# Kernel tuning notes

Hardware: AMD Instinct MI355X
Metric: run time of the kernel (lower is better)

Reference implementation:

```python
import jax, jax.numpy as jnp
import numpy as np

N = 100000          # nodes
E = 1600000         # edges
F_IN = 128          # in_channels
C = 32              # hidden_channels (per head)
H = 4               # heads
NEG_SLOPE = 0.2     # PyG GATConv default leaky_relu slope


def setup_inputs() -> dict:
    key = jax.random.key(0)
    ks = jax.random.split(key, 6)
    x = jax.random.normal(ks[0], (N, F_IN), dtype=jnp.float32)
    edge_index = jax.random.randint(ks[1], (2, E), 0, N, dtype=jnp.int32)
    # learned params (PyG GATConv: lin weight, att_src, att_dst, bias)
    W = jax.random.normal(ks[2], (F_IN, H * C), dtype=jnp.float32) * (1.0 / np.sqrt(F_IN))
    att_src = jax.random.normal(ks[3], (H, C), dtype=jnp.float32) * 0.1
    att_dst = jax.random.normal(ks[4], (H, C), dtype=jnp.float32) * 0.1
    bias = jnp.zeros((H * C,), dtype=jnp.float32)
    return {"x": x, "edge_index": edge_index, "W": W,
            "att_src": att_src, "att_dst": att_dst, "bias": bias}


def reference(x, edge_index, W, att_src, att_dst, bias):
    # linear projection, split into heads: [N, H, C]
    h = (x @ W).reshape(N, H, C)
    # per-node attention terms: [N, H]
    a_src = jnp.einsum('nhc,hc->nh', h, att_src)
    a_dst = jnp.einsum('nhc,hc->nh', h, att_dst)
    src, dst = edge_index[0], edge_index[1]
    # edge-wise logits: [E, H]
    alpha = jax.nn.leaky_relu(a_src[src] + a_dst[dst], NEG_SLOPE)
    # segment softmax over incoming edges of each dst node
    amax = jax.ops.segment_max(alpha, dst, num_segments=N)       # [N, H]
    amax = jnp.where(jnp.isfinite(amax), amax, 0.0)
    ex = jnp.exp(alpha - amax[dst])                              # [E, H]
    denom = jax.ops.segment_sum(ex, dst, num_segments=N)         # [N, H]
    alpha = ex / (denom[dst] + 1e-16)                            # [E, H]
    # weighted messages, scatter-add to dst: [N, H, C]
    msg = h[src] * alpha[:, :, None]
    out = jax.ops.segment_sum(msg, dst, num_segments=N)
    out = out.reshape(N, H * C) + bias
    return jax.nn.elu(out)
```

## Files before the change

kernel.cpp:

```cpp
#include <hip/hip_runtime.h>
#include <hip/hip_bf16.h>
#include <math.h>

#define N_NODES 100000
#define N_EDGES 1600000
#define NEG_SLOPE 0.2f

#define NB_BUCKET 782
#define ST_CAP 2560

#define OFF_H     0
#define OFF_ASRC  25600000
#define OFF_ADST  27200000
#define OFF_OFFS  28800000
#define OFF_BCNT  29200128
#define OFF_BOFF  29204224
#define OFF_BCUR  29208320
#define OFF_TMP   29212416
#define OFF_CSR   35612416

__device__ __forceinline__ float leaky(float x) {
    return fmaxf(x, NEG_SLOPE * x);
}
__device__ __forceinline__ float sel4(int h, float a, float b, float c, float d) {
    return h == 0 ? a : (h == 1 ? b : (h == 2 ? c : d));
}

#define BR 64
#define KT 32
__global__ __launch_bounds__(256, 4) void gemm_att_kernel(
    const float* __restrict__ x, const float* __restrict__ W,
    const float* __restrict__ att_src, const float* __restrict__ att_dst,
    __hip_bfloat162* __restrict__ h_bf, float* __restrict__ a_src,
    float* __restrict__ a_dst)
{
    __shared__ float xs[KT][68];
    __shared__ float ws[KT][132];

    const int tid = threadIdx.x;
    const int cx  = tid & 31;
    const int ry  = tid >> 5;
    const int n0  = blockIdx.x * BR;

    float acc[8][4];
#pragma unroll
    for (int i = 0; i < 8; ++i)
#pragma unroll
        for (int j = 0; j < 4; ++j) acc[i][j] = 0.f;

    const int sr  = tid >> 3;
    const int skk = (tid & 7) * 4;
    const int wc4 = (tid & 31) * 4;
    const int wk  = tid >> 5;

    for (int k0 = 0; k0 < 128; k0 += KT) {
#pragma unroll
        for (int rr = 0; rr < BR; rr += 32) {
            int row = n0 + sr + rr;
            row = row < N_NODES ? row : N_NODES - 1;
            const float4 v = *(const float4*)&x[(size_t)row * 128 + k0 + skk];
            xs[skk + 0][sr + rr] = v.x;
            xs[skk + 1][sr + rr] = v.y;
            xs[skk + 2][sr + rr] = v.z;
            xs[skk + 3][sr + rr] = v.w;
        }
#pragma unroll
        for (int kk2 = 0; kk2 < KT; kk2 += 8) {
            const float4 wv = *(const float4*)&W[(size_t)(k0 + wk + kk2) * 128 + wc4];
            *(float4*)&ws[wk + kk2][wc4] = wv;
        }
        __syncthreads();

#pragma unroll 4
        for (int k = 0; k < KT; ++k) {
            const float4 wv = *(const float4*)&ws[k][cx * 4];
            const float4 xa = *(const float4*)&xs[k][ry * 8];
            const float4 xb = *(const float4*)&xs[k][ry * 8 + 4];
            const float xr[8] = {xa.x, xa.y, xa.z, xa.w, xb.x, xb.y, xb.z, xb.w};
            const float wr[4] = {wv.x, wv.y, wv.z, wv.w};
#pragma unroll
            for (int i = 0; i < 8; ++i)
#pragma unroll
                for (int j = 0; j < 4; ++j)
                    acc[i][j] = fmaf(xr[i], wr[j], acc[i][j]);
        }
        __syncthreads();
    }

    const float4 as4 = ((const float4*)att_src)[cx];
    const float4 ad4 = ((const float4*)att_dst)[cx];
    const int hd = cx >> 3;

#pragma unroll
    for (int i = 0; i < 8; ++i) {
        const int row = n0 + ry * 8 + i;
        if (row >= N_NODES) break;
        union { __hip_bfloat162 h2[2]; uint2 u2; } pk;
        pk.h2[0].x = __float2bfloat16(acc[i][0]);
        pk.h2[0].y = __float2bfloat16(acc[i][1]);
        pk.h2[1].x = __float2bfloat16(acc[i][2]);
        pk.h2[1].y = __float2bfloat16(acc[i][3]);
        ((uint2*)h_bf)[(size_t)row * 32 + cx] = pk.u2;

        float vs = acc[i][0] * as4.x + acc[i][1] * as4.y + acc[i][2] * as4.z + acc[i][3] * as4.w;
        float vd = acc[i][0] * ad4.x + acc[i][1] * ad4.y + acc[i][2] * ad4.z + acc[i][3] * ad4.w;
#pragma unroll
        for (int off = 1; off < 8; off <<= 1) {
            vs += __shfl_xor(vs, off);
            vd += __shfl_xor(vd, off);
        }
        if ((cx & 7) == 0) {
            a_src[row * 4 + hd] = vs;
            a_dst[row * 4 + hd] = vd;
        }
    }
}

#define BH_EPB 6250
__global__ __launch_bounds__(256) void bucket_hist_kernel(
    const int* __restrict__ dst, int* __restrict__ bcnt)
{
    __shared__ int cnt[NB_BUCKET];
    const int tid = threadIdx.x;
    for (int i = tid; i < NB_BUCKET; i += 256) cnt[i] = 0;
    __syncthreads();
    const int e0 = blockIdx.x * BH_EPB;
    for (int i = tid; i < BH_EPB; i += 256)
        atomicAdd(&cnt[dst[e0 + i] >> 7], 1);
    __syncthreads();
    for (int i = tid; i < NB_BUCKET; i += 256)
        if (cnt[i]) atomicAdd(&bcnt[i], cnt[i]);
}

__global__ __launch_bounds__(1024) void bucket_scan_kernel(
    const int* __restrict__ bcnt, int* __restrict__ boff, int* __restrict__ bcur)
{
    const int tid  = threadIdx.x;
    const int lane = tid & 63;
    const int wv   = tid >> 6;
    const int v    = (tid < NB_BUCKET) ? bcnt[tid] : 0;

    int sv = v;
#pragma unroll
    for (int off = 1; off < 64; off <<= 1) {
        int u = __shfl_up(sv, off);
        if (lane >= off) sv += u;
    }
    __shared__ int wsum[16];
    if (lane == 63) wsum[wv] = sv;
    __syncthreads();
    if (tid == 0) {
        int run = 0;
#pragma unroll
        for (int k = 0; k < 16; ++k) { int t = wsum[k]; wsum[k] = run; run += t; }
    }
    __syncthreads();
    if (tid < NB_BUCKET) {
        const int excl = wsum[wv] + sv - v;
        boff[tid] = excl;
        bcur[tid] = excl;
    }
    if (tid == 0) boff[NB_BUCKET] = N_EDGES;
}

#define S1_EPB 12500
__global__ __launch_bounds__(256) void scat1_kernel(
    const int* __restrict__ src, const int* __restrict__ dst,
    int* __restrict__ bcur, unsigned int* __restrict__ tmp)
{
    __shared__ int cnt[NB_BUCKET];
    const int tid = threadIdx.x;
    for (int i = tid; i < NB_BUCKET; i += 256) cnt[i] = 0;
    __syncthreads();
    const int e0 = blockIdx.x * S1_EPB;
    for (int i = tid; i < S1_EPB; i += 256)
        atomicAdd(&cnt[dst[e0 + i] >> 7], 1);
    __syncthreads();
    for (int b = tid; b < NB_BUCKET; b += 256) {
        const int c = cnt[b];
        cnt[b] = c ? atomicAdd(&bcur[b], c) : 0;
    }
    __syncthreads();
    for (int i = tid; i < S1_EPB; i += 256) {
        const int d = dst[e0 + i];
        const int s = src[e0 + i];
        const int p = atomicAdd(&cnt[d >> 7], 1);
        tmp[p] = ((unsigned int)s << 7) | (unsigned int)(d & 127);
    }
}

__global__ __launch_bounds__(256) void phaseB_kernel(
    const unsigned int* __restrict__ tmp, const int* __restrict__ boff,
    int* __restrict__ offs, int* __restrict__ csr)
{
    __shared__ unsigned int st[ST_CAP];
    __shared__ int hist[128];
    __shared__ int cur[128];
    __shared__ int wtot[4];

    const int b    = blockIdx.x;
    const int tid  = threadIdx.x;
    const int lane = tid & 63;
    const int wv   = tid >> 6;
    const int base = boff[b];
    const int cnt  = boff[b + 1] - base;

    if (tid < 128) hist[tid] = 0;
    __syncthreads();

    for (int i = tid; i < cnt; i += 256) {
        const unsigned int v = tmp[base + i];
        if (i < ST_CAP) st[i] = v;
        atomicAdd(&hist[v & 127], 1);
    }
    __syncthreads();

    const int hv = (tid < 128) ? hist[tid] : 0;
    int sv = hv;
#pragma unroll
    for (int off = 1; off < 64; off <<= 1) {
        int u = __shfl_up(sv, off);
        if (lane >= off) sv += u;
    }
    if (lane == 63) wtot[wv] = sv;
    __syncthreads();
    const int wpre = (wv > 0 ? wtot[0] : 0) + (wv > 1 ? wtot[1] : 0) + (wv > 2 ? wtot[2] : 0);
    if (tid < 128) {
        const int excl = wpre + sv - hv;
        cur[tid] = excl;
        const int node = (b << 7) + tid;
        if (node < N_NODES) offs[node] = base + excl;
    }
    if (b == 0 && tid == 0) offs[N_NODES] = N_EDGES;
    __syncthreads();

    for (int i = tid; i < cnt; i += 256) {
        const unsigned int v = (i < ST_CAP) ? st[i] : tmp[base + i];
        const int p = atomicAdd(&cur[v & 127], 1);
        csr[base + p] = (int)(v >> 7);
    }
}

__global__ __launch_bounds__(256, 4) void gat_agg_kernel(
    const int* __restrict__ csr_src, const int* __restrict__ offs,
    const __hip_bfloat162* __restrict__ h_bf,
    const float* __restrict__ a_src, const float* __restrict__ a_dst,
    const float* __restrict__ bias, float* __restrict__ out)
{
    __shared__ float4 stage[4][128];

    const int wv   = threadIdx.x >> 6;
    const int lane = threadIdx.x & 63;
    const int node = blockIdx.x * 4 + wv;
    const int hidx = lane >> 4;

    const int start = offs[node];
    const int deg   = offs[node + 1] - start;

    const float4 ad4 = ((const float4*)a_dst)[node];

    float sf = __int_as_float(0);
    float e0 = 0.f, e1 = 0.f, e2 = 0.f, e3 = 0.f;
    if (lane < deg) {
        const int s = csr_src[start + lane];
        sf = __int_as_float(s);
        const float4 as4 = ((const float4*)a_src)[s];
        e0 = __expf(leaky(as4.x + ad4.x));
        e1 = __expf(leaky(as4.y + ad4.y));
        e2 = __expf(leaky(as4.z + ad4.z));
        e3 = __expf(leaky(as4.w + ad4.w));
    }
    stage[wv][lane * 2 + 0] = make_float4(sf, e0, sf, e1);
    stage[wv][lane * 2 + 1] = make_float4(sf, e2, sf, e3);
    __syncthreads();

    float2 acc = {0.f, 0.f};
    float  den = 0.f;
    const float2* sp = (const float2*)&stage[wv][0];

    if (deg <= 64) {
        int j = 0;
        for (; j + 4 <= deg; j += 4) {
            const float2 v0 = sp[(j + 0) * 4 + hidx];
            const float2 v1 = sp[(j + 1) * 4 + hidx];
            const float2 v2 = sp[(j + 2) * 4 + hidx];
            const float2 v3 = sp[(j + 3) * 4 + hidx];
            const int s0 = __float_as_int(v0.x);
            const int s1 = __float_as_int(v1.x);
            const int s2 = __float_as_int(v2.x);
            const int s3 = __float_as_int(v3.x);
            const __hip_bfloat162 hb0 = h_bf[(size_t)s0 * 64 + lane];
            const __hip_bfloat162 hb1 = h_bf[(size_t)s1 * 64 + lane];
            const __hip_bfloat162 hb2 = h_bf[(size_t)s2 * 64 + lane];
            const __hip_bfloat162 hb3 = h_bf[(size_t)s3 * 64 + lane];
            const float2 f0 = __bfloat1622float2(hb0);
            const float2 f1 = __bfloat1622float2(hb1);
            const float2 f2 = __bfloat1622float2(hb2);
            const float2 f3 = __bfloat1622float2(hb3);
            acc.x += v0.y * f0.x + v1.y * f1.x + v2.y * f2.x + v3.y * f3.x;
            acc.y += v0.y * f0.y + v1.y * f1.y + v2.y * f2.y + v3.y * f3.y;
            den   += v0.y + v1.y + v2.y + v3.y;
        }
        for (; j < deg; ++j) {
            const float2 v = sp[j * 4 + hidx];
            const int s = __float_as_int(v.x);
            const float2 f = __bfloat1622float2(h_bf[(size_t)s * 64 + lane]);
            acc.x += v.y * f.x;
            acc.y += v.y * f.y;
            den   += v.y;
        }
    } else {
        const float adh = sel4(hidx, ad4.x, ad4.y, ad4.z, ad4.w);
        for (int j = 0; j < deg; ++j) {
            const int s = csr_src[start + j];
            const float ash = a_src[s * 4 + hidx];
            const float ex = __expf(leaky(ash + adh));
            const float2 f = __bfloat1622float2(h_bf[(size_t)s * 64 + lane]);
            acc.x += ex * f.x;
            acc.y += ex * f.y;
            den   += ex;
        }
    }

    const float inv = 1.0f / (den + 1e-16f);
    const float2 b2 = ((const float2*)bias)[lane];
    float ox = acc.x * inv + b2.x;
    float oy = acc.y * inv + b2.y;
    ox = ox > 0.f ? ox : expm1f(ox);
    oy = oy > 0.f ? oy : expm1f(oy);
    ((float2*)out)[(size_t)node * 64 + lane] = make_float2(ox, oy);
}

extern "C" void kernel_launch(void* const* d_in, const int* in_sizes, int n_in,
                              void* d_out, int out_size, void* d_ws, size_t ws_size,
                              hipStream_t stream)
{
    const float* x       = (const float*)d_in[0];
    const int*   ei      = (const int*)  d_in[1];
    const float* W       = (const float*)d_in[2];
    const float* att_src = (const float*)d_in[3];
    const float* att_dst = (const float*)d_in[4];
    const float* bias    = (const float*)d_in[5];
    float*       out     = (float*)d_out;

    char* ws = (char*)d_ws;
    __hip_bfloat162* h_bf = (__hip_bfloat162*)(ws + OFF_H);
    float* a_src = (float*)(ws + OFF_ASRC);
    float* a_dst = (float*)(ws + OFF_ADST);
    int*   offs  = (int*)  (ws + OFF_OFFS);
    int*   bcnt  = (int*)  (ws + OFF_BCNT);
    int*   boff  = (int*)  (ws + OFF_BOFF);
    int*   bcur  = (int*)  (ws + OFF_BCUR);
    unsigned int* tmp = (unsigned int*)(ws + OFF_TMP);
    int*   csr   = (int*)  (ws + OFF_CSR);

    const int* srcp = ei;
    const int* dstp = ei + N_EDGES;

    hipMemsetAsync(bcnt, 0, NB_BUCKET * sizeof(int), stream);

    gemm_att_kernel<<<(N_NODES + BR - 1) / BR, 256, 0, stream>>>(
        x, W, att_src, att_dst, h_bf, a_src, a_dst);

    bucket_hist_kernel<<<N_EDGES / BH_EPB, 256, 0, stream>>>(dstp, bcnt);
    bucket_scan_kernel<<<1, 1024, 0, stream>>>(bcnt, boff, bcur);
    scat1_kernel<<<N_EDGES / S1_EPB, 256, 0, stream>>>(srcp, dstp, bcur, tmp);
    phaseB_kernel<<<NB_BUCKET, 256, 0, stream>>>(tmp, boff, offs, csr);

    gat_agg_kernel<<<N_NODES / 4, 256, 0, stream>>>(
        csr, offs, h_bf, a_src, a_dst, bias, out);
}
```

Baseline: 293.1 us.

## Widen GEMM tile and gather 16-byte bf16 rows across four edges in aggregation

The projection GEMM moves to a 128-row block with an 8x8 register tile per thread and writes h as packed uint4 bf16. The aggregation kernel now processes four edges in parallel per wavefront, each 16-lane group loading a full 16-byte chunk, then reduces partial sums with shuffles. High-degree nodes are handled by chunked staging instead of a serial fallback. The bucket histogram and scatter kernels use smaller per-block edge counts, giving more blocks. The larger GEMM tile raises register pressure, and block-wide syncs across chunk loops may cause imbalance between waves.

```diff
diff --git a/kernel.cpp b/kernel.cpp
--- a/kernel.cpp
+++ b/kernel.cpp
@@ -22,101 +22,122 @@
 __device__ __forceinline__ float leaky(float x) {
     return fmaxf(x, NEG_SLOPE * x);
 }
-__device__ __forceinline__ float sel4(int h, float a, float b, float c, float d) {
-    return h == 0 ? a : (h == 1 ? b : (h == 2 ? c : d));
-}
-
-#define BR 64
-#define KT 32
-__global__ __launch_bounds__(256, 4) void gemm_att_kernel(
+__device__ __forceinline__ unsigned int pack_bf2(float a, float b) {
+    unsigned int ua = (unsigned int)__bfloat16_as_ushort(__float2bfloat16(a));
+    unsigned int ub = (unsigned int)__bfloat16_as_ushort(__float2bfloat16(b));
+    return ua | (ub << 16);
+}
+__device__ __forceinline__ float bf_lo(unsigned int u) {
+    return __uint_as_float(u << 16);
+}
+__device__ __forceinline__ float bf_hi(unsigned int u) {
+    return __uint_as_float(u & 0xffff0000u);
+}
+
+#define BR2 128
+__global__ __launch_bounds__(256, 2) void gemm_att_kernel(
     const float* __restrict__ x, const float* __restrict__ W,
     const float* __restrict__ att_src, const float* __restrict__ att_dst,
-    __hip_bfloat162* __restrict__ h_bf, float* __restrict__ a_src,
-    float* __restrict__ a_dst)
-{
-    __shared__ float xs[KT][68];
-    __shared__ float ws[KT][132];
+    uint4* __restrict__ h4, float* __restrict__ a_src, float* __restrict__ a_dst)
+{
+    __shared__ float xs[32][BR2 + 4];
+    __shared__ float ws[32][132];
 
     const int tid = threadIdx.x;
-    const int cx  = tid & 31;
-    const int ry  = tid >> 5;
-    const int n0  = blockIdx.x * BR;
-
-    float acc[8][4];
+    const int cx  = tid & 15;
+    const int ry  = tid >> 4;
+    const int n0  = blockIdx.x * BR2;
+
+    float acc[8][8];
 #pragma unroll
     for (int i = 0; i < 8; ++i)
 #pragma unroll
-        for (int j = 0; j < 4; ++j) acc[i][j] = 0.f;
-
-    const int sr  = tid >> 3;
-    const int skk = (tid & 7) * 4;
-    const int wc4 = (tid & 31) * 4;
-    const int wk  = tid >> 5;
-
-    for (int k0 = 0; k0 < 128; k0 += KT) {
-#pragma unroll
-        for (int rr = 0; rr < BR; rr += 32) {
-            int row = n0 + sr + rr;
+        for (int j = 0; j < 8; ++j) acc[i][j] = 0.f;
+
+    const int xr  = tid >> 1;
+    const int xk0 = (tid & 1) * 16;
+    const int wk  = tid >> 3;
+    const int wc0 = (tid & 7) * 16;
+
+    for (int k0 = 0; k0 < 128; k0 += 32) {
+        {
+            int row = n0 + xr;
             row = row < N_NODES ? row : N_NODES - 1;
-            const float4 v = *(const float4*)&x[(size_t)row * 128 + k0 + skk];
-            xs[skk + 0][sr + rr] = v.x;
-            xs[skk + 1][sr + rr] = v.y;
-            xs[skk + 2][sr + rr] = v.z;
-            xs[skk + 3][sr + rr] = v.w;
-        }
-#pragma unroll
-        for (int kk2 = 0; kk2 < KT; kk2 += 8) {
-            const float4 wv = *(const float4*)&W[(size_t)(k0 + wk + kk2) * 128 + wc4];
-            *(float4*)&ws[wk + kk2][wc4] = wv;
+            const float4* xp = (const float4*)&x[(size_t)row * 128 + k0 + xk0];
+#pragma unroll
+            for (int i = 0; i < 4; ++i) {
+                const float4 v = xp[i];
+                xs[xk0 + i * 4 + 0][xr] = v.x;
+                xs[xk0 + i * 4 + 1][xr] = v.y;
+                xs[xk0 + i * 4 + 2][xr] = v.z;
+                xs[xk0 + i * 4 + 3][xr] = v.w;
+            }
+        }
+        {
+            const float4* wp = (const float4*)&W[(size_t)(k0 + wk) * 128 + wc0];
+#pragma unroll
+            for (int i = 0; i < 4; ++i)
+                *(float4*)&ws[wk][wc0 + i * 4] = wp[i];
         }
         __syncthreads();
 
-#pragma unroll 4
-        for (int k = 0; k < KT; ++k) {
-            const float4 wv = *(const float4*)&ws[k][cx * 4];
+#pragma unroll 2
+        for (int k = 0; k < 32; ++k) {
             const float4 xa = *(const float4*)&xs[k][ry * 8];
             const float4 xb = *(const float4*)&xs[k][ry * 8 + 4];
-            const float xr[8] = {xa.x, xa.y, xa.z, xa.w, xb.x, xb.y, xb.z, xb.w};
-            const float wr[4] = {wv.x, wv.y, wv.z, wv.w};
+            const float4 wa = *(const float4*)&ws[k][cx * 8];
+            const float4 wb = *(const float4*)&ws[k][cx * 8 + 4];
+            const float xv[8] = {xa.x, xa.y, xa.z, xa.w, xb.x, xb.y, xb.z, xb.w};
+            const float wv[8] = {wa.x, wa.y, wa.z, wa.w, wb.x, wb.y, wb.z, wb.w};
 #pragma unroll
             for (int i = 0; i < 8; ++i)
 #pragma unroll
-                for (int j = 0; j < 4; ++j)
-                    acc[i][j] = fmaf(xr[i], wr[j], acc[i][j]);
+                for (int j = 0; j < 8; ++j)
+                    acc[i][j] = fmaf(xv[i], wv[j], acc[i][j]);
         }
         __syncthreads();
     }
 
-    const float4 as4 = ((const float4*)att_src)[cx];
-    const float4 ad4 = ((const float4*)att_dst)[cx];
-    const int hd = cx >> 3;
+    float as8[8], ad8[8];
+    {
+        const float4 a0 = ((const float4*)att_src)[cx * 2];
+        const float4 a1 = ((const float4*)att_src)[cx * 2 + 1];
+        const float4 b0 = ((const float4*)att_dst)[cx * 2];
+        const float4 b1 = ((const float4*)att_dst)[cx * 2 + 1];
+        as8[0]=a0.x; as8[1]=a0.y; as8[2]=a0.z; as8[3]=a0.w;
+        as8[4]=a1.x; as8[5]=a1.y; as8[6]=a1.z; as8[7]=a1.w;
+        ad8[0]=b0.x; ad8[1]=b0.y; ad8[2]=b0.z; ad8[3]=b0.w;
+        ad8[4]=b1.x; ad8[5]=b1.y; ad8[6]=b1.z; ad8[7]=b1.w;
+    }
+    const int head = cx >> 2;
 
 #pragma unroll
     for (int i = 0; i < 8; ++i) {
         const int row = n0 + ry * 8 + i;
         if (row >= N_NODES) break;
-        union { __hip_bfloat162 h2[2]; uint2 u2; } pk;
-        pk.h2[0].x = __float2bfloat16(acc[i][0]);
-        pk.h2[0].y = __float2bfloat16(acc[i][1]);
-        pk.h2[1].x = __float2bfloat16(acc[i][2]);
-        pk.h2[1].y = __float2bfloat16(acc[i][3]);
-        ((uint2*)h_bf)[(size_t)row * 32 + cx] = pk.u2;
-
-        float vs = acc[i][0] * as4.x + acc[i][1] * as4.y + acc[i][2] * as4.z + acc[i][3] * as4.w;
-        float vd = acc[i][0] * ad4.x + acc[i][1] * ad4.y + acc[i][2] * ad4.z + acc[i][3] * ad4.w;
-#pragma unroll
-        for (int off = 1; off < 8; off <<= 1) {
-            vs += __shfl_xor(vs, off);
-            vd += __shfl_xor(vd, off);
-        }
-        if ((cx & 7) == 0) {
-            a_src[row * 4 + hd] = vs;
-            a_dst[row * 4 + hd] = vd;
-        }
-    }
-}
-
-#define BH_EPB 6250
+        uint4 pk;
+        pk.x = pack_bf2(acc[i][0], acc[i][1]);
+        pk.y = pack_bf2(acc[i][2], acc[i][3]);
+        pk.z = pack_bf2(acc[i][4], acc[i][5]);
+        pk.w = pack_bf2(acc[i][6], acc[i][7]);
+        h4[(size_t)row * 16 + cx] = pk;
+
+        float vs = 0.f, vd = 0.f;
+#pragma unroll
+        for (int c = 0; c < 8; ++c) {
+            vs = fmaf(acc[i][c], as8[c], vs);
+            vd = fmaf(acc[i][c], ad8[c], vd);
+        }
+        vs += __shfl_xor(vs, 1); vd += __shfl_xor(vd, 1);
+        vs += __shfl_xor(vs, 2); vd += __shfl_xor(vd, 2);
+        if ((cx & 3) == 0) {
+            a_src[row * 4 + head] = vs;
+            a_dst[row * 4 + head] = vd;
+        }
+    }
+}
+
+#define BH_EPB 3125
 __global__ __launch_bounds__(256) void bucket_hist_kernel(
     const int* __restrict__ dst, int* __restrict__ bcnt)
 {
@@ -163,7 +184,7 @@
     if (tid == 0) boff[NB_BUCKET] = N_EDGES;
 }
 
-#define S1_EPB 12500
+#define S1_EPB 3125
 __global__ __launch_bounds__(256) void scat1_kernel(
     const int* __restrict__ src, const int* __restrict__ dst,
     int* __restrict__ bcur, unsigned int* __restrict__ tmp)
@@ -224,7 +245,7 @@
     }
     if (lane == 63) wtot[wv] = sv;
     __syncthreads();
-    const int wpre = (wv > 0 ? wtot[0] : 0) + (wv > 1 ? wtot[1] : 0) + (wv > 2 ? wtot[2] : 0);
+    const int wpre = (wv > 0 ? wtot[0] : 0) + (wv > 1 ? wtot[1] : 0);
     if (tid < 128) {
         const int excl = wpre + sv - hv;
         cur[tid] = excl;
@@ -241,94 +262,100 @@
     }
 }
 
-__global__ __launch_bounds__(256, 4) void gat_agg_kernel(
+__global__ __launch_bounds__(256) void gat_agg_kernel(
     const int* __restrict__ csr_src, const int* __restrict__ offs,
-    const __hip_bfloat162* __restrict__ h_bf,
+    const uint4* __restrict__ h4,
     const float* __restrict__ a_src, const float* __restrict__ a_dst,
     const float* __restrict__ bias, float* __restrict__ out)
 {
-    __shared__ float4 stage[4][128];
+    __shared__ float2 st[4][4][68];
+    __shared__ int s_nch[4];
 
     const int wv   = threadIdx.x >> 6;
     const int lane = threadIdx.x & 63;
     const int node = blockIdx.x * 4 + wv;
-    const int hidx = lane >> 4;
+    const int q    = lane >> 4;
+    const int l16  = lane & 15;
+    const int hq   = l16 >> 2;
 
     const int start = offs[node];
     const int deg   = offs[node + 1] - start;
-
     const float4 ad4 = ((const float4*)a_dst)[node];
 
-    float sf = __int_as_float(0);
-    float e0 = 0.f, e1 = 0.f, e2 = 0.f, e3 = 0.f;
-    if (lane < deg) {
-        const int s = csr_src[start + lane];
-        sf = __int_as_float(s);
-        const float4 as4 = ((const float4*)a_src)[s];
-        e0 = __expf(leaky(as4.x + ad4.x));
-        e1 = __expf(leaky(as4.y + ad4.y));
-        e2 = __expf(leaky(as4.z + ad4.z));
-        e3 = __expf(leaky(as4.w + ad4.w));
-    }
-    stage[wv][lane * 2 + 0] = make_float4(sf, e0, sf, e1);
-    stage[wv][lane * 2 + 1] = make_float4(sf, e2, sf, e3);
-    __syncthreads();
-
-    float2 acc = {0.f, 0.f};
-    float  den = 0.f;
-    const float2* sp = (const float2*)&stage[wv][0];
-
-    if (deg <= 64) {
-        int j = 0;
-        for (; j + 4 <= deg; j += 4) {
-            const float2 v0 = sp[(j + 0) * 4 + hidx];
-            const float2 v1 = sp[(j + 1) * 4 + hidx];
-            const float2 v2 = sp[(j + 2) * 4 + hidx];
-            const float2 v3 = sp[(j + 3) * 4 + hidx];
-            const int s0 = __float_as_int(v0.x);
-            const int s1 = __float_as_int(v1.x);
-            const int s2 = __float_as_int(v2.x);
-            const int s3 = __float_as_int(v3.x);
-            const __hip_bfloat162 hb0 = h_bf[(size_t)s0 * 64 + lane];
-            const __hip_bfloat162 hb1 = h_bf[(size_t)s1 * 64 + lane];
-            const __hip_bfloat162 hb2 = h_bf[(size_t)s2 * 64 + lane];
-            const __hip_bfloat162 hb3 = h_bf[(size_t)s3 * 64 + lane];
-            const float2 f0 = __bfloat1622float2(hb0);
-            const float2 f1 = __bfloat1622float2(hb1);
-            const float2 f2 = __bfloat1622float2(hb2);
-            const float2 f3 = __bfloat1622float2(hb3);
-            acc.x += v0.y * f0.x + v1.y * f1.x + v2.y * f2.x + v3.y * f3.x;
-            acc.y += v0.y * f0.y + v1.y * f1.y + v2.y * f2.y + v3.y * f3.y;
-            den   += v0.y + v1.y + v2.y + v3.y;
-        }
-        for (; j < deg; ++j) {
-            const float2 v = sp[j * 4 + hidx];
-            const int s = __float_as_int(v.x);
-            const float2 f = __bfloat1622float2(h_bf[(size_t)s * 64 + lane]);
-            acc.x += v.y * f.x;
-            acc.y += v.y * f.y;
-            den   += v.y;
-        }
-    } else {
-        const float adh = sel4(hidx, ad4.x, ad4.y, ad4.z, ad4.w);
-        for (int j = 0; j < deg; ++j) {
-            const int s = csr_src[start + j];
-            const float ash = a_src[s * 4 + hidx];
-            const float ex = __expf(leaky(ash + adh));
-            const float2 f = __bfloat1622float2(h_bf[(size_t)s * 64 + lane]);
-            acc.x += ex * f.x;
-            acc.y += ex * f.y;
-            den   += ex;
-        }
-    }
-
-    const float inv = 1.0f / (den + 1e-16f);
-    const float2 b2 = ((const float2*)bias)[lane];
-    float ox = acc.x * inv + b2.x;
-    float oy = acc.y * inv + b2.y;
-    ox = ox > 0.f ? ox : expm1f(ox);
-    oy = oy > 0.f ? oy : expm1f(oy);
-    ((float2*)out)[(size_t)node * 64 + lane] = make_float2(ox, oy);
+    if (lane == 0) s_nch[wv] = (deg + 63) >> 6;
+    __syncthreads();
+    const int cmax = max(max(s_nch[0], s_nch[1]), max(s_nch[2], s_nch[3]));
+
+    float acc[8];
+#pragma unroll
+    for (int c = 0; c < 8; ++c) acc[c] = 0.f;
+    float den = 0.f;
+
+    for (int ch = 0; ch < cmax; ++ch) {
+        const int base = ch << 6;
+        const int rem  = deg - base;
+
+        float sf = 0.f, e0 = 0.f, e1 = 0.f, e2 = 0.f, e3 = 0.f;
+        if (lane < rem) {
+            const int s = csr_src[start + base + lane];
+            sf = __int_as_float(s);
+            const float4 as4 = ((const float4*)a_src)[s];
+            e0 = __expf(leaky(as4.x + ad4.x));
+            e1 = __expf(leaky(as4.y + ad4.y));
+            e2 = __expf(leaky(as4.z + ad4.z));
+            e3 = __expf(leaky(as4.w + ad4.w));
+        }
+        st[wv][0][lane] = make_float2(sf, e0);
+        st[wv][1][lane] = make_float2(sf, e1);
+        st[wv][2][lane] = make_float2(sf, e2);
+        st[wv][3][lane] = make_float2(sf, e3);
+        __syncthreads();
+
+        const int cnt4 = rem > 0 ? ((rem > 64 ? 64 : (rem + 3) & ~3)) : 0;
+        const float2* sp = &st[wv][hq][q];
+        for (int j = 0; j < cnt4; j += 4) {
+            const float2 se = sp[j];
+            const unsigned int soff =
+                (__float_as_uint(se.x) << 4) + (unsigned int)l16;
+            const uint4 hv = h4[soff];
+            const float ex = se.y;
+            acc[0] = fmaf(bf_lo(hv.x), ex, acc[0]);
+            acc[1] = fmaf(bf_hi(hv.x), ex, acc[1]);
+            acc[2] = fmaf(bf_lo(hv.y), ex, acc[2]);
+            acc[3] = fmaf(bf_hi(hv.y), ex, acc[3]);
+            acc[4] = fmaf(bf_lo(hv.z), ex, acc[4]);
+            acc[5] = fmaf(bf_hi(hv.z), ex, acc[5]);
+            acc[6] = fmaf(bf_lo(hv.w), ex, acc[6]);
+            acc[7] = fmaf(bf_hi(hv.w), ex, acc[7]);
+            den += ex;
+        }
+        __syncthreads();
+    }
+
+#pragma unroll
+    for (int c = 0; c < 8; ++c) {
+        acc[c] += __shfl_xor(acc[c], 16);
+        acc[c] += __shfl_xor(acc[c], 32);
+    }
+    den += __shfl_xor(den, 16);
+    den += __shfl_xor(den, 32);
+
+    if (q == 0) {
+        const float inv = 1.0f / (den + 1e-16f);
+        const float4 b0 = ((const float4*)bias)[l16 * 2];
+        const float4 b1 = ((const float4*)bias)[l16 * 2 + 1];
+        float o[8];
+        o[0] = acc[0] * inv + b0.x; o[1] = acc[1] * inv + b0.y;
+        o[2] = acc[2] * inv + b0.z; o[3] = acc[3] * inv + b0.w;
+        o[4] = acc[4] * inv + b1.x; o[5] = acc[5] * inv + b1.y;
+        o[6] = acc[6] * inv + b1.z; o[7] = acc[7] * inv + b1.w;
+#pragma unroll
+        for (int c = 0; c < 8; ++c)
+            o[c] = o[c] > 0.f ? o[c] : expm1f(o[c]);
+        float4* op = (float4*)&out[(size_t)node * 128 + l16 * 8];
+        op[0] = make_float4(o[0], o[1], o[2], o[3]);
+        op[1] = make_float4(o[4], o[5], o[6], o[7]);
+    }
 }
 
 extern "C" void kernel_launch(void* const* d_in, const int* in_sizes, int n_in,
@@ -344,7 +371,7 @@
     float*       out     = (float*)d_out;
 
     char* ws = (char*)d_ws;
-    __hip_bfloat162* h_bf = (__hip_bfloat162*)(ws + OFF_H);
+    uint4* h4    = (uint4*)(ws + OFF_H);
     float* a_src = (float*)(ws + OFF_ASRC);
     float* a_dst = (float*)(ws + OFF_ADST);
     int*   offs  = (int*)  (ws + OFF_OFFS);
@@ -359,8 +386,8 @@
 
     hipMemsetAsync(bcnt, 0, NB_BUCKET * sizeof(int), stream);
 
-    gemm_att_kernel<<<(N_NODES + BR - 1) / BR, 256, 0, stream>>>(
-        x, W, att_src, att_dst, h_bf, a_src, a_dst);
+    gemm_att_kernel<<<(N_NODES + BR2 - 1) / BR2, 256, 0, stream>>>(
+        x, W, att_src, att_dst, h4, a_src, a_dst);
 
     bucket_hist_kernel<<<N_EDGES / BH_EPB, 256, 0, stream>>>(dstp, bcnt);
     bucket_scan_kernel<<<1, 1024, 0, stream>>>(bcnt, boff, bcur);
@@ -368,5 +395,5 @@
     phaseB_kernel<<<NB_BUCKET, 256, 0, stream>>>(tmp, boff, offs, csr);
 
     gat_agg_kernel<<<N_NODES / 4, 256, 0, stream>>>(
-        csr, offs, h_bf, a_src, a_dst, bias, out);
-}
+        csr, offs, h4, a_src, a_dst, bias, out);
+}
```

After: 300.1 us. 2.4% more time.
